# Optimization experiments

Measured on AMD Instinct MI355X. Metric: run time of the kernel, lower is better.

Reference implementation:

```python
import jax, jax.numpy as jnp
import numpy as np

N = 12288


def setup_inputs() -> dict:
    key = jax.random.key(0)
    k = jax.random.split(key, 6)
    return {
        "params": jax.random.normal(k[0], (N,), dtype=jnp.float32),
        "triggers": jax.random.uniform(k[1], (N,), dtype=jnp.float32),
        "r_mask": jax.random.uniform(k[2], (N,), dtype=jnp.float32),
        "ics_mask": jax.random.uniform(k[3], (N,), dtype=jnp.float32),
        "vcsw_mask": jax.random.uniform(k[4], (N,), dtype=jnp.float32),
        "vc_mask": jax.random.uniform(k[5], (N,), dtype=jnp.float32),
    }


def reference(params, triggers, r_mask, ics_mask, vcsw_mask, vc_mask):
    # Original torch code: -diag(params)@diag(r_mask) + diag(ics_mask)
    #                      + diag(triggers)@diag(vcsw_mask) + diag(vc_mask)
    # diag(a)@diag(b) == diag(a*b), so the whole expression is a single
    # diagonal matrix built from one fused elementwise vector expression.
    d = -params * r_mask + ics_mask + triggers * vcsw_mask + vc_mask  # [n]
    return jnp.diag(d)  # [n, n]
```

## Files before the change

kernel.cpp:

```cpp
#include <hip/hip_runtime.h>

static constexpr int N = 12288;
static constexpr int F4_PER_ROW = N / 4;
static constexpr int BLOCK = 256;
static constexpr int BLOCKS_PER_ROW = F4_PER_ROW / BLOCK;

typedef float vfloat4 __attribute__((ext_vector_type(4)));

__global__ __launch_bounds__(BLOCK)
void impedance_fused_kernel(const float* __restrict__ params,
                            const float* __restrict__ triggers,
                            const float* __restrict__ r_mask,
                            const float* __restrict__ ics_mask,
                            const float* __restrict__ vcsw_mask,
                            const float* __restrict__ vc_mask,
                            float* __restrict__ out) {
    const int row = blockIdx.y;
    const int c4  = blockIdx.x * BLOCK + threadIdx.x;

    vfloat4 v = (vfloat4)(0.f);
    if (c4 == (row >> 2)) {
        float d = fmaf(-params[row], r_mask[row],
                  fmaf(triggers[row], vcsw_mask[row],
                       ics_mask[row] + vc_mask[row]));
        v[row & 3] = d;
    }

    vfloat4* dst = (vfloat4*)(out + (size_t)row * N) + c4;
    __builtin_nontemporal_store(v, dst);
}

extern "C" void kernel_launch(void* const* d_in, const int* in_sizes, int n_in,
                              void* d_out, int out_size, void* d_ws, size_t ws_size,
                              hipStream_t stream) {
    const float* params    = (const float*)d_in[0];
    const float* triggers  = (const float*)d_in[1];
    const float* r_mask    = (const float*)d_in[2];
    const float* ics_mask  = (const float*)d_in[3];
    const float* vcsw_mask = (const float*)d_in[4];
    const float* vc_mask   = (const float*)d_in[5];
    float* out = (float*)d_out;

    dim3 grid(BLOCKS_PER_ROW, N, 1);
    dim3 block(BLOCK, 1, 1);
    impedance_fused_kernel<<<grid, block, 0, stream>>>(
        params, triggers, r_mask, ics_mask, vcsw_mask, vc_mask, out);
}
```

Baseline: 97.26 us.

## Zero output with hipMemsetAsync and scatter diagonal in a small kernel

Replaces the fused kernel, which wrote every float4 of the dense matrix and computed the diagonal inline, with a runtime memset that zeroes the whole output followed by a tiny kernel that writes only the N diagonal entries. The aim is to use the driver's fill path for the 600MB zero fill and keep the compute kernel trivial. This adds a second launch and scattered single-float diagonal writes, and whether the measured kernel time covers the memset depends on the harness.

Result: slower. 102.6 us (+5.5%).

```diff
diff --git a/kernel.cpp b/kernel.cpp
--- a/kernel.cpp
+++ b/kernel.cpp
@@ -1,33 +1,22 @@
 #include <hip/hip_runtime.h>
 
 static constexpr int N = 12288;
-static constexpr int F4_PER_ROW = N / 4;
-static constexpr int BLOCK = 256;
-static constexpr int BLOCKS_PER_ROW = F4_PER_ROW / BLOCK;
+static constexpr int DIAG_BLOCK = 256;
+static constexpr int DIAG_GRID = N / DIAG_BLOCK;
 
-typedef float vfloat4 __attribute__((ext_vector_type(4)));
-
-__global__ __launch_bounds__(BLOCK)
-void impedance_fused_kernel(const float* __restrict__ params,
-                            const float* __restrict__ triggers,
-                            const float* __restrict__ r_mask,
-                            const float* __restrict__ ics_mask,
-                            const float* __restrict__ vcsw_mask,
-                            const float* __restrict__ vc_mask,
-                            float* __restrict__ out) {
-    const int row = blockIdx.y;
-    const int c4  = blockIdx.x * BLOCK + threadIdx.x;
-
-    vfloat4 v = (vfloat4)(0.f);
-    if (c4 == (row >> 2)) {
-        float d = fmaf(-params[row], r_mask[row],
-                  fmaf(triggers[row], vcsw_mask[row],
-                       ics_mask[row] + vc_mask[row]));
-        v[row & 3] = d;
-    }
-
-    vfloat4* dst = (vfloat4*)(out + (size_t)row * N) + c4;
-    __builtin_nontemporal_store(v, dst);
+__global__ __launch_bounds__(DIAG_BLOCK)
+void impedance_diag_kernel(const float* __restrict__ params,
+                           const float* __restrict__ triggers,
+                           const float* __restrict__ r_mask,
+                           const float* __restrict__ ics_mask,
+                           const float* __restrict__ vcsw_mask,
+                           const float* __restrict__ vc_mask,
+                           float* __restrict__ out) {
+    const int i = blockIdx.x * DIAG_BLOCK + threadIdx.x;
+    const float d = fmaf(-params[i], r_mask[i],
+                    fmaf(triggers[i], vcsw_mask[i],
+                         ics_mask[i] + vc_mask[i]));
+    out[(size_t)i * (N + 1)] = d;
 }
 
 extern "C" void kernel_launch(void* const* d_in, const int* in_sizes, int n_in,
@@ -41,8 +30,10 @@
     const float* vc_mask   = (const float*)d_in[5];
     float* out = (float*)d_out;
 
-    dim3 grid(BLOCKS_PER_ROW, N, 1);
-    dim3 block(BLOCK, 1, 1);
-    impedance_fused_kernel<<<grid, block, 0, stream>>>(
+    hipMemsetAsync(out, 0, (size_t)N * N * sizeof(float), stream);
+
+    dim3 grid(DIAG_GRID, 1, 1);
+    dim3 block(DIAG_BLOCK, 1, 1);
+    impedance_diag_kernel<<<grid, block, 0, stream>>>(
         params, triggers, r_mask, ics_mask, vcsw_mask, vc_mask, out);
 }
```
